# Performance work log

Hardware: AMD Instinct MI355X
Metric: run time of the kernel (lower is better)

The kernel has to match this reference:

```python
import jax, jax.numpy as jnp
import numpy as np

N, E, DIN, DH, DOUT = 50000, 800000, 128, 128, 64


def setup_inputs() -> dict:
    key = jax.random.key(0)
    ks = jax.random.split(key, 10)
    s = 0.05  # keep activations numerically sane
    return {
        "x": jax.random.normal(ks[0], (N, DIN), jnp.float32),
        "edge_index": jax.random.randint(ks[1], (2, E), 0, N, jnp.int64),
        "w_in": jax.random.normal(ks[2], (DIN, DH), jnp.float32) * s,
        "b_in": jnp.zeros((DH,), jnp.float32),
        "w_l0": jax.random.normal(ks[3], (DH, DH), jnp.float32) * s,
        "w_r0": jax.random.normal(ks[4], (DH, DH), jnp.float32) * s,
        "b0": jnp.zeros((DH,), jnp.float32),
        "w_l1": jax.random.normal(ks[5], (DH, DH), jnp.float32) * s,
        "w_r1": jax.random.normal(ks[6], (DH, DH), jnp.float32) * s,
        "b1": jnp.zeros((DH,), jnp.float32),
        "w_l2": jax.random.normal(ks[7], (DH, DOUT), jnp.float32) * s,
        "w_r2": jax.random.normal(ks[8], (DH, DOUT), jnp.float32) * s,
        "b2": jnp.zeros((DOUT,), jnp.float32),
    }


def _sage_conv(x, src, dst, w_l, w_r, b, n_nodes):
    # PyG SAGEConv (mean aggr): out = lin_l(mean_{j in N(i)} x_j) + lin_r(x_i)
    msg = x[src]  # [E, d] gather
    agg = jax.ops.segment_sum(msg, dst, num_segments=n_nodes)
    deg = jax.ops.segment_sum(jnp.ones((src.shape[0],), x.dtype), dst, num_segments=n_nodes)
    agg = agg / jnp.maximum(deg, 1.0)[:, None]  # isolated nodes -> 0
    return agg @ w_l + x @ w_r + b


def reference(x, edge_index, w_in, b_in, w_l0, w_r0, b0, w_l1, w_r1, b1, w_l2, w_r2, b2):
    src, dst = edge_index[0], edge_index[1]
    n = x.shape[0]
    h = x @ w_in + b_in
    inp = h
    h = jax.nn.relu(h)
    # conv 0 (hidden->hidden) + relu + (eval dropout = id) + residual
    h = _sage_conv(h, src, dst, w_l0, w_r0, b0, n)
    h = jax.nn.relu(h) + 0.2 * inp
    # conv 1 (hidden->hidden)
    h = _sage_conv(h, src, dst, w_l1, w_r1, b1, n)
    h = jax.nn.relu(h) + 0.2 * inp
    # conv 2 (hidden->out), no activation/residual
    h = _sage_conv(h, src, dst, w_l2, w_r2, b2, n)
    return jax.nn.log_softmax(h, axis=-1)
```

## Files before the change

kernel.cpp:

```cpp
#include <hip/hip_runtime.h>
#include <stdint.h>

#define NN 50000
#define NE 800000
#define NBIN 196
#define ABLK 196
#define EPB 4082
#define BCAP 6144

typedef __attribute__((ext_vector_type(8))) short short8;
typedef __attribute__((ext_vector_type(4))) float floatx4;

__device__ __forceinline__ uint16_t f2bf(float f){
  union { float f; uint32_t u; } c; c.f = f;
  uint32_t u = c.u + 0x7FFFu + ((c.u >> 16) & 1u);
  return (uint16_t)(u >> 16);
}
__device__ __forceinline__ float bflo(uint32_t v){
  union { uint32_t u; float f; } c; c.u = v << 16; return c.f;
}
__device__ __forceinline__ float bfhi(uint32_t v){
  union { uint32_t u; float f; } c; c.u = v & 0xFFFF0000u; return c.f;
}

#define B_HIST ABLK
#define B_PIN 64
#define B_P0  128
#define B_P1  128
#define B_P2  64

__device__ __forceinline__ void pack_one(int idx, const float* __restrict__ wl,
                                         const float* __restrict__ wr,
                                         uint16_t* __restrict__ bp,
                                         int ncolL, int ncolR, int NT){
  int j = idx & 7, lane = (idx >> 3) & 63, rest = idx >> 9;
  int nt = rest % NT, kt = rest / NT;
  int k = kt * 32 + ((lane >> 4) << 3) + j;
  int n = nt * 16 + (lane & 15);
  float v = (n < ncolL) ? wl[k * ncolL + n] : wr[k * ncolR + (n - ncolL)];
  bp[idx] = f2bf(v);
}

__global__ __launch_bounds__(256) void k_prep(const int* __restrict__ ei, int* __restrict__ histG,
                                              const float* __restrict__ w_in,
                                              const float* __restrict__ w_l0, const float* __restrict__ w_r0,
                                              const float* __restrict__ w_l1, const float* __restrict__ w_r1,
                                              const float* __restrict__ w_l2, const float* __restrict__ w_r2,
                                              uint16_t* __restrict__ bpIn, uint16_t* __restrict__ bp0,
                                              uint16_t* __restrict__ bp1, uint16_t* __restrict__ bp2){
  __shared__ int hsh[NBIN];
  int b = blockIdx.x;
  if (b < B_HIST){
    for (int i = threadIdx.x; i < NBIN; i += 256) hsh[i] = 0;
    __syncthreads();
    int base = b * EPB;
    for (int k = threadIdx.x; k < EPB; k += 256){
      int e = base + k;
      if (e < NE) atomicAdd(&hsh[ei[NE + e] >> 8], 1);
    }
    __syncthreads();
    for (int i = threadIdx.x; i < NBIN; i += 256) histG[b * NBIN + i] = hsh[i];
    return;
  }
  b -= B_HIST;
  if (b < B_PIN){ pack_one(b * 256 + threadIdx.x, w_in, w_in, bpIn, 128, 0, 8); return; }
  b -= B_PIN;
  if (b < B_P0){ pack_one(b * 256 + threadIdx.x, w_l0, w_r0, bp0, 128, 128, 16); return; }
  b -= B_P0;
  if (b < B_P1){ pack_one(b * 256 + threadIdx.x, w_l1, w_r1, bp1, 128, 128, 16); return; }
  b -= B_P1;
  pack_one(b * 256 + threadIdx.x, w_l2, w_r2, bp2, 64, 64, 8);
}

__global__ __launch_bounds__(256) void k_scanS1(int* __restrict__ histG, int* __restrict__ colTot){
  __shared__ int s[256];
  int t = blockIdx.x;
  int b = threadIdx.x;
  int v = (b < ABLK) ? histG[b * NBIN + t] : 0;
  s[b] = v;
  __syncthreads();
  #pragma unroll
  for (int off = 1; off < 256; off <<= 1){
    int u = (b >= off) ? s[b - off] : 0;
    __syncthreads();
    s[b] += u;
    __syncthreads();
  }
  if (b < ABLK) histG[b * NBIN + t] = s[b] - v;
  if (b == ABLK - 1) colTot[t] = s[b];
}

__global__ __launch_bounds__(256) void k_scanS2(const int* __restrict__ colTot, int* __restrict__ binStart){
  __shared__ int s[256];
  int t = threadIdx.x;
  int tot = (t < NBIN) ? colTot[t] : 0;
  s[t] = tot;
  __syncthreads();
  #pragma unroll
  for (int off = 1; off < 256; off <<= 1){
    int u = (t >= off) ? s[t - off] : 0;
    __syncthreads();
    s[t] += u;
    __syncthreads();
  }
  if (t < NBIN) binStart[t] = s[t] - tot;
  if (t == 0) binStart[NBIN] = NE;
}

#define B_BIN 196
#define SMSZ 20488

__global__ __launch_bounds__(256) void k_mid(const int* __restrict__ ei, const int* __restrict__ histG,
                                             const int* __restrict__ binStart,
                                             uint32_t* __restrict__ pairs,
                                             const float* __restrict__ x,
                                             const uint16_t* __restrict__ BpIn, const float* __restrict__ b_in,
                                             const uint16_t* __restrict__ Bp0, const float* __restrict__ b0,
                                             uint16_t* __restrict__ resb, uint16_t* __restrict__ y0,
                                             uint16_t* __restrict__ z0){
  __shared__ __align__(16) char smraw[SMSZ];
  int t = threadIdx.x;
  if (blockIdx.x < B_BIN){
    int* h   = (int*)smraw;
    int* loc = h + NBIN;
    int* cur = loc + NBIN;
    int* gof = cur + NBIN;
    int* sc  = gof + NBIN;
    uint32_t* st = (uint32_t*)(sc + 256);
    int base = blockIdx.x * EPB;
    for (int i = t; i < NBIN; i += 256) h[i] = 0;
    __syncthreads();
    for (int k = t; k < EPB; k += 256){
      int e = base + k;
      if (e < NE) atomicAdd(&h[ei[NE + e] >> 8], 1);
    }
    __syncthreads();
    int cv = (t < NBIN) ? h[t] : 0;
    sc[t] = cv;
    __syncthreads();
    #pragma unroll
    for (int off = 1; off < 256; off <<= 1){
      int u = (t >= off) ? sc[t - off] : 0;
      __syncthreads();
      sc[t] += u;
      __syncthreads();
    }
    if (t < NBIN){
      int excl = sc[t] - cv;
      loc[t] = excl;
      cur[t] = excl;
      gof[t] = binStart[t] + histG[blockIdx.x * NBIN + t];
    }
    __syncthreads();
    for (int k = t; k < EPB; k += 256){
      int e = base + k;
      if (e < NE){
        int d = ei[NE + e];
        int s0 = ei[e];
        int pos = atomicAdd(&cur[d >> 8], 1);
        st[pos] = (uint32_t)s0 | ((uint32_t)d << 16);
      }
    }
    __syncthreads();
    int cnt = min(EPB, NE - base);
    for (int k = t; k < cnt; k += 256){
      uint32_t v = st[k];
      int bin = (int)(v >> 24);
      pairs[gof[bin] + (k - loc[bin])] = v;
    }
    return;
  }
  uint16_t* ash = (uint16_t*)smraw;
  int lane = t & 63, wave = t >> 6;
  short8 bIn[4][2], bC0[4][4];
  #pragma unroll
  for (int kt = 0; kt < 4; ++kt){
    #pragma unroll
    for (int n = 0; n < 2; ++n)
      bIn[kt][n] = *(const short8*)(BpIn + (size_t)((kt * 8 + wave * 2 + n) * 64 + lane) * 8);
    #pragma unroll
    for (int n = 0; n < 4; ++n)
      bC0[kt][n] = *(const short8*)(Bp0 + (size_t)((kt * 16 + wave * 4 + n) * 64 + lane) * 8);
  }
  int m = lane & 15, quad = lane >> 4;
  int r0 = (blockIdx.x - B_BIN) * 16;
  const float* xrow = x + (size_t)(r0 + m) * 128 + quad * 8;
  short8 af[4];
  #pragma unroll
  for (int kt = 0; kt < 4; ++kt){
    float4 p = *(const float4*)(xrow + kt * 32);
    float4 q2 = *(const float4*)(xrow + kt * 32 + 4);
    short8 a;
    a[0] = (short)f2bf(p.x);  a[1] = (short)f2bf(p.y);
    a[2] = (short)f2bf(p.z);  a[3] = (short)f2bf(p.w);
    a[4] = (short)f2bf(q2.x); a[5] = (short)f2bf(q2.y);
    a[6] = (short)f2bf(q2.z); a[7] = (short)f2bf(q2.w);
    af[kt] = a;
  }
  floatx4 accH[2];
  #pragma unroll
  for (int n = 0; n < 2; ++n) accH[n] = (floatx4){0.f, 0.f, 0.f, 0.f};
  #pragma unroll
  for (int kt = 0; kt < 4; ++kt)
    #pragma unroll
    for (int n = 0; n < 2; ++n)
      accH[n] = __builtin_amdgcn_mfma_f32_16x16x32_bf16(af[kt], bIn[kt][n], accH[n], 0, 0, 0);
  int rbase = r0 + quad * 4;
  #pragma unroll
  for (int n = 0; n < 2; ++n){
    int c = (wave * 2 + n) * 16 + m;
    float bi = b_in[c];
    #pragma unroll
    for (int i = 0; i < 4; ++i){
      float hh = accH[n][i] + bi;
      int row = rbase + i;
      resb[(size_t)row * 128 + c] = f2bf(0.2f * hh);
      ash[(quad * 4 + i) * 136 + c] = f2bf(fmaxf(hh, 0.f));
    }
  }
  __syncthreads();
  short8 af2[4];
  #pragma unroll
  for (int kt = 0; kt < 4; ++kt)
    af2[kt] = *(const short8*)&ash[m * 136 + quad * 8 + kt * 32];
  floatx4 acc[4];
  #pragma unroll
  for (int n = 0; n < 4; ++n) acc[n] = (floatx4){0.f, 0.f, 0.f, 0.f};
  #pragma unroll
  for (int kt = 0; kt < 4; ++kt)
    #pragma unroll
    for (int n = 0; n < 4; ++n)
      acc[n] = __builtin_amdgcn_mfma_f32_16x16x32_bf16(af2[kt], bC0[kt][n], acc[n], 0, 0, 0);
  #pragma unroll
  for (int n = 0; n < 4; ++n){
    int c = (wave * 4 + n) * 16 + m;
    #pragma unroll
    for (int i = 0; i < 4; ++i){
      float v = acc[n][i];
      int row = rbase + i;
      if (c < 128) y0[(size_t)row * 128 + c] = f2bf(v);
      else         z0[(size_t)row * 128 + (c - 128)] = f2bf(v + b0[c - 128]);
    }
  }
}

__global__ __launch_bounds__(256) void k_csr(const uint32_t* __restrict__ pairs, const int* __restrict__ binStart,
                                             int* __restrict__ rowp, uint16_t* __restrict__ colx){
  __shared__ uint32_t pl[BCAP];
  __shared__ uint16_t stg[BCAP];
  __shared__ int h[256], sc[256];
  int i = blockIdx.x, t = threadIdx.x;
  int p0 = binStart[i], p1 = binStart[i + 1];
  int cnt = min(p1 - p0, BCAP);
  for (int k = t; k < cnt; k += 256) pl[k] = pairs[p0 + k];
  h[t] = 0;
  __syncthreads();
  for (int k = t; k < cnt; k += 256) atomicAdd(&h[(pl[k] >> 16) & 255], 1);
  __syncthreads();
  int cv = h[t];
  sc[t] = cv;
  __syncthreads();
  #pragma unroll
  for (int off = 1; off < 256; off <<= 1){
    int u = (t >= off) ? sc[t - off] : 0;
    __syncthreads();
    sc[t] += u;
    __syncthreads();
  }
  int excl = sc[t] - cv;
  int n0 = i << 8;
  int nc = min(256, NN - n0);
  if (t < nc) rowp[n0 + t] = p0 + excl;
  if (i == NBIN - 1 && t == 0) rowp[NN] = NE;
  h[t] = excl;
  __syncthreads();
  for (int k = t; k < cnt; k += 256){
    uint32_t v = pl[k];
    int pos = atomicAdd(&h[(v >> 16) & 255], 1);
    stg[pos] = (uint16_t)(v & 0xFFFFu);
  }
  __syncthreads();
  for (int k = t; k < cnt; k += 256) colx[p0 + k] = stg[k];
}

template<int NTW, int MODE>
__global__ __launch_bounds__(256) void k_gemm(const uint16_t* __restrict__ A, const uint16_t* __restrict__ Bp,
                                              const float* __restrict__ bias,
                                              uint16_t* __restrict__ o0, uint16_t* __restrict__ o1,
                                              float* __restrict__ o2){
  const int NTT = 4 * NTW;
  int lane = threadIdx.x & 63;
  int wave = threadIdx.x >> 6;
  short8 bfrag[4][NTW];
  #pragma unroll
  for (int kt = 0; kt < 4; ++kt)
    #pragma unroll
    for (int n = 0; n < NTW; ++n)
      bfrag[kt][n] = *(const short8*)(Bp + (size_t)((kt * NTT + wave * NTW + n) * 64 + lane) * 8);

  int m = lane & 15, quad = lane >> 4;
  const int nrt = NN / 16;
  for (int rt = blockIdx.x; rt < nrt; rt += gridDim.x){
    int r0 = rt * 16;
    const uint16_t* arow = A + (size_t)(r0 + m) * 128 + quad * 8;
    short8 af[4];
    #pragma unroll
    for (int kt = 0; kt < 4; ++kt) af[kt] = *(const short8*)(arow + kt * 32);
    floatx4 acc[NTW];
    #pragma unroll
    for (int n = 0; n < NTW; ++n) acc[n] = (floatx4){0.f, 0.f, 0.f, 0.f};
    #pragma unroll
    for (int kt = 0; kt < 4; ++kt)
      #pragma unroll
      for (int n = 0; n < NTW; ++n)
        acc[n] = __builtin_amdgcn_mfma_f32_16x16x32_bf16(af[kt], bfrag[kt][n], acc[n], 0, 0, 0);

    int rbase = r0 + quad * 4;
    #pragma unroll
    for (int n = 0; n < NTW; ++n){
      int c = (wave * NTW + n) * 16 + m;
      #pragma unroll
      for (int i = 0; i < 4; ++i){
        float v = acc[n][i];
        int row = rbase + i;
        if (MODE == 1){
          if (c < 128) o0[(size_t)row * 128 + c] = f2bf(v);
          else         o1[(size_t)row * 128 + (c - 128)] = f2bf(v + bias[c - 128]);
        } else {
          if (c < 64) o0[(size_t)row * 64 + c] = f2bf(v);
          else        o2[(size_t)row * 64 + (c - 64)] = v + bias[c - 64];
        }
      }
    }
  }
}

__global__ __launch_bounds__(256) void agg_mid(const uint4* __restrict__ yb, const uint4* __restrict__ zb,
                                               const uint4* __restrict__ resb,
                                               const uint16_t* __restrict__ colx, const int* __restrict__ rowp,
                                               uint4* __restrict__ hb_out){
  int wid = blockIdx.x * 4 + (threadIdx.x >> 6);
  if (wid >= NN) return;
  int lane = threadIdx.x & 63;
  int q = lane >> 4, sub = lane & 15;
  int e0 = rowp[wid], e1 = rowp[wid + 1];
  float a0 = 0.f, a1 = 0.f, a2 = 0.f, a3 = 0.f, a4 = 0.f, a5 = 0.f, a6 = 0.f, a7 = 0.f;
  int e = e0 + q;
  for (; e + 12 < e1; e += 16){
    uint4 v0 = yb[(size_t)colx[e]      * 16 + sub];
    uint4 v1 = yb[(size_t)colx[e + 4]  * 16 + sub];
    uint4 v2 = yb[(size_t)colx[e + 8]  * 16 + sub];
    uint4 v3 = yb[(size_t)colx[e + 12] * 16 + sub];
    a0 += bflo(v0.x) + bflo(v1.x) + bflo(v2.x) + bflo(v3.x);
    a1 += bfhi(v0.x) + bfhi(v1.x) + bfhi(v2.x) + bfhi(v3.x);
    a2 += bflo(v0.y) + bflo(v1.y) + bflo(v2.y) + bflo(v3.y);
    a3 += bfhi(v0.y) + bfhi(v1.y) + bfhi(v2.y) + bfhi(v3.y);
    a4 += bflo(v0.z) + bflo(v1.z) + bflo(v2.z) + bflo(v3.z);
    a5 += bfhi(v0.z) + bfhi(v1.z) + bfhi(v2.z) + bfhi(v3.z);
    a6 += bflo(v0.w) + bflo(v1.w) + bflo(v2.w) + bflo(v3.w);
    a7 += bfhi(v0.w) + bfhi(v1.w) + bfhi(v2.w) + bfhi(v3.w);
  }
  for (; e < e1; e += 4){
    uint4 v = yb[(size_t)colx[e] * 16 + sub];
    a0 += bflo(v.x); a1 += bfhi(v.x); a2 += bflo(v.y); a3 += bfhi(v.y);
    a4 += bflo(v.z); a5 += bfhi(v.z); a6 += bflo(v.w); a7 += bfhi(v.w);
  }
  #pragma unroll
  for (int off = 16; off < 64; off <<= 1){
    a0 += __shfl_xor(a0, off, 64);
    a1 += __shfl_xor(a1, off, 64);
    a2 += __shfl_xor(a2, off, 64);
    a3 += __shfl_xor(a3, off, 64);
    a4 += __shfl_xor(a4, off, 64);
    a5 += __shfl_xor(a5, off, 64);
    a6 += __shfl_xor(a6, off, 64);
    a7 += __shfl_xor(a7, off, 64);
  }
  int deg = e1 - e0;
  float inv = deg > 0 ? 1.f / (float)deg : 0.f;
  if (q == 0){
    uint4 zv = zb[(size_t)wid * 16 + sub];
    uint4 rv = resb[(size_t)wid * 16 + sub];
    float w0 = fmaxf(a0 * inv + bflo(zv.x), 0.f) + bflo(rv.x);
    float w1 = fmaxf(a1 * inv + bfhi(zv.x), 0.f) + bfhi(rv.x);
    float w2 = fmaxf(a2 * inv + bflo(zv.y), 0.f) + bflo(rv.y);
    float w3 = fmaxf(a3 * inv + bfhi(zv.y), 0.f) + bfhi(rv.y);
    float w4 = fmaxf(a4 * inv + bflo(zv.z), 0.f) + bflo(rv.z);
    float w5 = fmaxf(a5 * inv + bfhi(zv.z), 0.f) + bfhi(rv.z);
    float w6 = fmaxf(a6 * inv + bflo(zv.w), 0.f) + bflo(rv.w);
    float w7 = fmaxf(a7 * inv + bfhi(zv.w), 0.f) + bfhi(rv.w);
    uint4 o;
    o.x = (uint32_t)f2bf(w0) | ((uint32_t)f2bf(w1) << 16);
    o.y = (uint32_t)f2bf(w2) | ((uint32_t)f2bf(w3) << 16);
    o.z = (uint32_t)f2bf(w4) | ((uint32_t)f2bf(w5) << 16);
    o.w = (uint32_t)f2bf(w6) | ((uint32_t)f2bf(w7) << 16);
    hb_out[(size_t)wid * 16 + sub] = o;
  }
}

__global__ __launch_bounds__(256) void agg_out(const uint2* __restrict__ yb2, const float* __restrict__ z2,
                                               const uint16_t* __restrict__ colx, const int* __restrict__ rowp,
                                               float* __restrict__ out){
  int wid = blockIdx.x * 4 + (threadIdx.x >> 6);
  if (wid >= NN) return;
  int lane = threadIdx.x & 63;
  int q = lane >> 4, sub = lane & 15;
  int e0 = rowp[wid], e1 = rowp[wid + 1];
  float a0 = 0.f, a1 = 0.f, a2 = 0.f, a3 = 0.f;
  int e = e0 + q;
  for (; e + 12 < e1; e += 16){
    uint2 v0 = yb2[(size_t)colx[e]      * 16 + sub];
    uint2 v1 = yb2[(size_t)colx[e + 4]  * 16 + sub];
    uint2 v2 = yb2[(size_t)colx[e + 8]  * 16 + sub];
    uint2 v3 = yb2[(size_t)colx[e + 12] * 16 + sub];
    a0 += bflo(v0.x) + bflo(v1.x) + bflo(v2.x) + bflo(v3.x);
    a1 += bfhi(v0.x) + bfhi(v1.x) + bfhi(v2.x) + bfhi(v3.x);
    a2 += bflo(v0.y) + bflo(v1.y) + bflo(v2.y) + bflo(v3.y);
    a3 += bfhi(v0.y) + bfhi(v1.y) + bfhi(v2.y) + bfhi(v3.y);
  }
  for (; e < e1; e += 4){
    uint2 v = yb2[(size_t)colx[e] * 16 + sub];
    a0 += bflo(v.x); a1 += bfhi(v.x); a2 += bflo(v.y); a3 += bfhi(v.y);
  }
  #pragma unroll
  for (int off = 16; off < 64; off <<= 1){
    a0 += __shfl_xor(a0, off, 64);
    a1 += __shfl_xor(a1, off, 64);
    a2 += __shfl_xor(a2, off, 64);
    a3 += __shfl_xor(a3, off, 64);
  }
  int deg = e1 - e0;
  float inv = deg > 0 ? 1.f / (float)deg : 0.f;
  float4 zv = ((const float4*)z2)[(size_t)wid * 16 + sub];
  float v0 = a0 * inv + zv.x;
  float v1 = a1 * inv + zv.y;
  float v2 = a2 * inv + zv.z;
  float v3 = a3 * inv + zv.w;
  float mx = fmaxf(fmaxf(v0, v1), fmaxf(v2, v3));
  #pragma unroll
  for (int off = 1; off < 16; off <<= 1) mx = fmaxf(mx, __shfl_xor(mx, off, 64));
  float sm = __expf(v0 - mx) + __expf(v1 - mx) + __expf(v2 - mx) + __expf(v3 - mx);
  #pragma unroll
  for (int off = 1; off < 16; off <<= 1) sm += __shfl_xor(sm, off, 64);
  if (q == 0){
    float ls = __logf(sm);
    float4 o = make_float4((v0 - mx) - ls, (v1 - mx) - ls, (v2 - mx) - ls, (v3 - mx) - ls);
    ((float4*)out)[(size_t)wid * 16 + sub] = o;
  }
}

extern "C" void kernel_launch(void* const* d_in, const int* in_sizes, int n_in,
                              void* d_out, int out_size, void* d_ws, size_t ws_size,
                              hipStream_t stream){
  const float* x    = (const float*)d_in[0];
  const int*   ei   = (const int*)d_in[1];
  const float* w_in = (const float*)d_in[2];
  const float* b_in = (const float*)d_in[3];
  const float* w_l0 = (const float*)d_in[4];
  const float* w_r0 = (const float*)d_in[5];
  const float* b0   = (const float*)d_in[6];
  const float* w_l1 = (const float*)d_in[7];
  const float* w_r1 = (const float*)d_in[8];
  const float* b1   = (const float*)d_in[9];
  const float* w_l2 = (const float*)d_in[10];
  const float* w_r2 = (const float*)d_in[11];
  const float* b2   = (const float*)d_in[12];
  float* out = (float*)d_out;

  char* ws = (char*)d_ws;
  size_t off = 0;
  auto take = [&](size_t bytes) -> char* {
    char* p = ws + off;
    off = (off + bytes + 1023) & ~(size_t)1023;
    return p;
  };
  uint16_t* hb   = (uint16_t*)take((size_t)NN * 128 * 2);
  uint16_t* resb = (uint16_t*)take((size_t)NN * 128 * 2);
  uint16_t* y0   = (uint16_t*)take((size_t)NN * 128 * 2);
  uint16_t* z0   = (uint16_t*)take((size_t)NN * 128 * 2);
  uint32_t* pairs = (uint32_t*)take((size_t)NE * 4);
  uint16_t* colx  = (uint16_t*)take((size_t)NE * 2);
  int* histG    = (int*)take((size_t)NBIN * ABLK * 4);
  int* colTot   = (int*)take((size_t)NBIN * 4);
  int* binStart = (int*)take((size_t)(NBIN + 1) * 4);
  int* rowp     = (int*)take((size_t)(NN + 1) * 4);
  uint16_t* BpIn = (uint16_t*)take(128 * 128 * 2);
  uint16_t* Bp0  = (uint16_t*)take(128 * 256 * 2);
  uint16_t* Bp1  = (uint16_t*)take(128 * 256 * 2);
  uint16_t* Bp2  = (uint16_t*)take(128 * 128 * 2);
  uint16_t* y2 = y0;
  float*    z2 = (float*)z0;
  (void)ws_size; (void)in_sizes; (void)n_in; (void)out_size;

  k_prep<<<B_HIST + B_PIN + B_P0 + B_P1 + B_P2, 256, 0, stream>>>(
      ei, histG, w_in, w_l0, w_r0, w_l1, w_r1, w_l2, w_r2, BpIn, Bp0, Bp1, Bp2);

  k_scanS1<<<NBIN, 256, 0, stream>>>(histG, colTot);
  k_scanS2<<<1, 256, 0, stream>>>(colTot, binStart);

  k_mid<<<B_BIN + NN / 16, 256, 0, stream>>>(ei, histG, binStart, pairs, x,
                                             BpIn, b_in, Bp0, b0, resb, y0, z0);

  k_csr<<<NBIN, 256, 0, stream>>>(pairs, binStart, rowp, colx);

  agg_mid<<<NN / 4, 256, 0, stream>>>((const uint4*)y0, (const uint4*)z0, (const uint4*)resb,
                                      colx, rowp, (uint4*)hb);
  k_gemm<4, 1><<<1024, 256, 0, stream>>>(hb, Bp1, b1, y0, z0, nullptr);

  agg_mid<<<NN / 4, 256, 0, stream>>>((const uint4*)y0, (const uint4*)z0, (const uint4*)resb,
                                      colx, rowp, (uint4*)hb);
  k_gemm<2, 2><<<1024, 256, 0, stream>>>(hb, Bp2, b2, y2, nullptr, z2);

  agg_out<<<NN / 4, 256, 0, stream>>>((const uint2*)y2, z2, colx, rowp, out);
}
```

Measured before the change: 274.7 us.

## Reuse prep histogram in binning and make linear blocks grid-stride persistent

The binning blocks in k_mid no longer recompute the per-block destination histogram over all edges. They read the raw counts saved by k_prep, which now goes to a separate histC buffer while the scan writes exclusive offsets to histE. The dense input/conv0 part of k_mid now runs 1024 persistent blocks in a grid-stride loop over row tiles instead of one block per tile. This amortises the per-block weight fragment loads, at the cost of an extra barrier per iteration and less parallelism.

```diff
diff --git a/kernel.cpp b/kernel.cpp
--- a/kernel.cpp
+++ b/kernel.cpp
@@ -7,6 +7,8 @@
 #define ABLK 196
 #define EPB 4082
 #define BCAP 6144
+#define NRT 3125
+#define GRID_LIN 1024
 
 typedef __attribute__((ext_vector_type(8))) short short8;
 typedef __attribute__((ext_vector_type(4))) float floatx4;
@@ -41,7 +43,7 @@
   bp[idx] = f2bf(v);
 }
 
-__global__ __launch_bounds__(256) void k_prep(const int* __restrict__ ei, int* __restrict__ histG,
+__global__ __launch_bounds__(256) void k_prep(const int* __restrict__ ei, int* __restrict__ histC,
                                               const float* __restrict__ w_in,
                                               const float* __restrict__ w_l0, const float* __restrict__ w_r0,
                                               const float* __restrict__ w_l1, const float* __restrict__ w_r1,
@@ -59,7 +61,7 @@
       if (e < NE) atomicAdd(&hsh[ei[NE + e] >> 8], 1);
     }
     __syncthreads();
-    for (int i = threadIdx.x; i < NBIN; i += 256) histG[b * NBIN + i] = hsh[i];
+    for (int i = threadIdx.x; i < NBIN; i += 256) histC[b * NBIN + i] = hsh[i];
     return;
   }
   b -= B_HIST;
@@ -72,11 +74,12 @@
   pack_one(b * 256 + threadIdx.x, w_l2, w_r2, bp2, 64, 64, 8);
 }
 
-__global__ __launch_bounds__(256) void k_scanS1(int* __restrict__ histG, int* __restrict__ colTot){
+__global__ __launch_bounds__(256) void k_scanS1(const int* __restrict__ histC, int* __restrict__ histE,
+                                                int* __restrict__ colTot){
   __shared__ int s[256];
   int t = blockIdx.x;
   int b = threadIdx.x;
-  int v = (b < ABLK) ? histG[b * NBIN + t] : 0;
+  int v = (b < ABLK) ? histC[b * NBIN + t] : 0;
   s[b] = v;
   __syncthreads();
   #pragma unroll
@@ -86,7 +89,7 @@
     s[b] += u;
     __syncthreads();
   }
-  if (b < ABLK) histG[b * NBIN + t] = s[b] - v;
+  if (b < ABLK) histE[b * NBIN + t] = s[b] - v;
   if (b == ABLK - 1) colTot[t] = s[b];
 }
 
@@ -110,7 +113,8 @@
 #define B_BIN 196
 #define SMSZ 20488
 
-__global__ __launch_bounds__(256) void k_mid(const int* __restrict__ ei, const int* __restrict__ histG,
+__global__ __launch_bounds__(256) void k_mid(const int* __restrict__ ei,
+                                             const int* __restrict__ histC, const int* __restrict__ histE,
                                              const int* __restrict__ binStart,
                                              uint32_t* __restrict__ pairs,
                                              const float* __restrict__ x,
@@ -121,21 +125,13 @@
   __shared__ __align__(16) char smraw[SMSZ];
   int t = threadIdx.x;
   if (blockIdx.x < B_BIN){
-    int* h   = (int*)smraw;
-    int* loc = h + NBIN;
+    int* loc = (int*)smraw;
     int* cur = loc + NBIN;
     int* gof = cur + NBIN;
-    int* sc  = gof + NBIN;
+    int* sc  = gof + NBIN + NBIN;
     uint32_t* st = (uint32_t*)(sc + 256);
-    int base = blockIdx.x * EPB;
-    for (int i = t; i < NBIN; i += 256) h[i] = 0;
-    __syncthreads();
-    for (int k = t; k < EPB; k += 256){
-      int e = base + k;
-      if (e < NE) atomicAdd(&h[ei[NE + e] >> 8], 1);
-    }
-    __syncthreads();
-    int cv = (t < NBIN) ? h[t] : 0;
+    int b = blockIdx.x;
+    int cv = (t < NBIN) ? histC[b * NBIN + t] : 0;
     sc[t] = cv;
     __syncthreads();
     #pragma unroll
@@ -149,9 +145,10 @@
       int excl = sc[t] - cv;
       loc[t] = excl;
       cur[t] = excl;
-      gof[t] = binStart[t] + histG[blockIdx.x * NBIN + t];
-    }
-    __syncthreads();
+      gof[t] = binStart[t] + histE[b * NBIN + t];
+    }
+    __syncthreads();
+    int base = b * EPB;
     for (int k = t; k < EPB; k += 256){
       int e = base + k;
       if (e < NE){
@@ -183,63 +180,66 @@
       bC0[kt][n] = *(const short8*)(Bp0 + (size_t)((kt * 16 + wave * 4 + n) * 64 + lane) * 8);
   }
   int m = lane & 15, quad = lane >> 4;
-  int r0 = (blockIdx.x - B_BIN) * 16;
-  const float* xrow = x + (size_t)(r0 + m) * 128 + quad * 8;
-  short8 af[4];
-  #pragma unroll
-  for (int kt = 0; kt < 4; ++kt){
-    float4 p = *(const float4*)(xrow + kt * 32);
-    float4 q2 = *(const float4*)(xrow + kt * 32 + 4);
-    short8 a;
-    a[0] = (short)f2bf(p.x);  a[1] = (short)f2bf(p.y);
-    a[2] = (short)f2bf(p.z);  a[3] = (short)f2bf(p.w);
-    a[4] = (short)f2bf(q2.x); a[5] = (short)f2bf(q2.y);
-    a[6] = (short)f2bf(q2.z); a[7] = (short)f2bf(q2.w);
-    af[kt] = a;
-  }
-  floatx4 accH[2];
-  #pragma unroll
-  for (int n = 0; n < 2; ++n) accH[n] = (floatx4){0.f, 0.f, 0.f, 0.f};
-  #pragma unroll
-  for (int kt = 0; kt < 4; ++kt)
-    #pragma unroll
-    for (int n = 0; n < 2; ++n)
-      accH[n] = __builtin_amdgcn_mfma_f32_16x16x32_bf16(af[kt], bIn[kt][n], accH[n], 0, 0, 0);
-  int rbase = r0 + quad * 4;
-  #pragma unroll
-  for (int n = 0; n < 2; ++n){
-    int c = (wave * 2 + n) * 16 + m;
-    float bi = b_in[c];
-    #pragma unroll
-    for (int i = 0; i < 4; ++i){
-      float hh = accH[n][i] + bi;
-      int row = rbase + i;
-      resb[(size_t)row * 128 + c] = f2bf(0.2f * hh);
-      ash[(quad * 4 + i) * 136 + c] = f2bf(fmaxf(hh, 0.f));
-    }
-  }
-  __syncthreads();
-  short8 af2[4];
-  #pragma unroll
-  for (int kt = 0; kt < 4; ++kt)
-    af2[kt] = *(const short8*)&ash[m * 136 + quad * 8 + kt * 32];
-  floatx4 acc[4];
-  #pragma unroll
-  for (int n = 0; n < 4; ++n) acc[n] = (floatx4){0.f, 0.f, 0.f, 0.f};
-  #pragma unroll
-  for (int kt = 0; kt < 4; ++kt)
-    #pragma unroll
-    for (int n = 0; n < 4; ++n)
-      acc[n] = __builtin_amdgcn_mfma_f32_16x16x32_bf16(af2[kt], bC0[kt][n], acc[n], 0, 0, 0);
-  #pragma unroll
-  for (int n = 0; n < 4; ++n){
-    int c = (wave * 4 + n) * 16 + m;
-    #pragma unroll
-    for (int i = 0; i < 4; ++i){
-      float v = acc[n][i];
-      int row = rbase + i;
-      if (c < 128) y0[(size_t)row * 128 + c] = f2bf(v);
-      else         z0[(size_t)row * 128 + (c - 128)] = f2bf(v + b0[c - 128]);
+  for (int rt = blockIdx.x - B_BIN; rt < NRT; rt += GRID_LIN){
+    int r0 = rt * 16;
+    const float* xrow = x + (size_t)(r0 + m) * 128 + quad * 8;
+    short8 af[4];
+    #pragma unroll
+    for (int kt = 0; kt < 4; ++kt){
+      float4 p = *(const float4*)(xrow + kt * 32);
+      float4 q2 = *(const float4*)(xrow + kt * 32 + 4);
+      short8 a;
+      a[0] = (short)f2bf(p.x);  a[1] = (short)f2bf(p.y);
+      a[2] = (short)f2bf(p.z);  a[3] = (short)f2bf(p.w);
+      a[4] = (short)f2bf(q2.x); a[5] = (short)f2bf(q2.y);
+      a[6] = (short)f2bf(q2.z); a[7] = (short)f2bf(q2.w);
+      af[kt] = a;
+    }
+    floatx4 accH[2];
+    #pragma unroll
+    for (int n = 0; n < 2; ++n) accH[n] = (floatx4){0.f, 0.f, 0.f, 0.f};
+    #pragma unroll
+    for (int kt = 0; kt < 4; ++kt)
+      #pragma unroll
+      for (int n = 0; n < 2; ++n)
+        accH[n] = __builtin_amdgcn_mfma_f32_16x16x32_bf16(af[kt], bIn[kt][n], accH[n], 0, 0, 0);
+    int rbase = r0 + quad * 4;
+    __syncthreads();
+    #pragma unroll
+    for (int n = 0; n < 2; ++n){
+      int c = (wave * 2 + n) * 16 + m;
+      float bi = b_in[c];
+      #pragma unroll
+      for (int i = 0; i < 4; ++i){
+        float hh = accH[n][i] + bi;
+        int row = rbase + i;
+        resb[(size_t)row * 128 + c] = f2bf(0.2f * hh);
+        ash[(quad * 4 + i) * 136 + c] = f2bf(fmaxf(hh, 0.f));
+      }
+    }
+    __syncthreads();
+    short8 af2[4];
+    #pragma unroll
+    for (int kt = 0; kt < 4; ++kt)
+      af2[kt] = *(const short8*)&ash[m * 136 + quad * 8 + kt * 32];
+    floatx4 acc[4];
+    #pragma unroll
+    for (int n = 0; n < 4; ++n) acc[n] = (floatx4){0.f, 0.f, 0.f, 0.f};
+    #pragma unroll
+    for (int kt = 0; kt < 4; ++kt)
+      #pragma unroll
+      for (int n = 0; n < 4; ++n)
+        acc[n] = __builtin_amdgcn_mfma_f32_16x16x32_bf16(af2[kt], bC0[kt][n], acc[n], 0, 0, 0);
+    #pragma unroll
+    for (int n = 0; n < 4; ++n){
+      int c = (wave * 4 + n) * 16 + m;
+      #pragma unroll
+      for (int i = 0; i < 4; ++i){
+        float v = acc[n][i];
+        int row = rbase + i;
+        if (c < 128) y0[(size_t)row * 128 + c] = f2bf(v);
+        else         z0[(size_t)row * 128 + (c - 128)] = f2bf(v + b0[c - 128]);
+      }
     }
   }
 }
@@ -480,7 +480,8 @@
   uint16_t* z0   = (uint16_t*)take((size_t)NN * 128 * 2);
   uint32_t* pairs = (uint32_t*)take((size_t)NE * 4);
   uint16_t* colx  = (uint16_t*)take((size_t)NE * 2);
-  int* histG    = (int*)take((size_t)NBIN * ABLK * 4);
+  int* histC    = (int*)take((size_t)NBIN * ABLK * 4);
+  int* histE    = (int*)take((size_t)NBIN * ABLK * 4);
   int* colTot   = (int*)take((size_t)NBIN * 4);
   int* binStart = (int*)take((size_t)(NBIN + 1) * 4);
   int* rowp     = (int*)take((size_t)(NN + 1) * 4);
@@ -493,13 +494,13 @@
   (void)ws_size; (void)in_sizes; (void)n_in; (void)out_size;
 
   k_prep<<<B_HIST + B_PIN + B_P0 + B_P1 + B_P2, 256, 0, stream>>>(
-      ei, histG, w_in, w_l0, w_r0, w_l1, w_r1, w_l2, w_r2, BpIn, Bp0, Bp1, Bp2);
-
-  k_scanS1<<<NBIN, 256, 0, stream>>>(histG, colTot);
+      ei, histC, w_in, w_l0, w_r0, w_l1, w_r1, w_l2, w_r2, BpIn, Bp0, Bp1, Bp2);
+
+  k_scanS1<<<NBIN, 256, 0, stream>>>(histC, histE, colTot);
   k_scanS2<<<1, 256, 0, stream>>>(colTot, binStart);
 
-  k_mid<<<B_BIN + NN / 16, 256, 0, stream>>>(ei, histG, binStart, pairs, x,
-                                             BpIn, b_in, Bp0, b0, resb, y0, z0);
+  k_mid<<<B_BIN + GRID_LIN, 256, 0, stream>>>(ei, histC, histE, binStart, pairs, x,
+                                              BpIn, b_in, Bp0, b0, resb, y0, z0);
 
   k_csr<<<NBIN, 256, 0, stream>>>(pairs, binStart, rowp, colx);
 
```

Measured after the change: 277.0 us. About the same (+0.8%).
